# Optimization experiments

Hardware: AMD Instinct MI355X
Metric: run time of the kernel (lower is better)

Reference implementation:

```python
import jax, jax.numpy as jnp
import numpy as np

B, C_IN, C_TMP, C_OUT, N = 4, 256, 256, 256, 4096


def setup_inputs() -> dict:
    key = jax.random.key(0)
    k1, k2, k3, k4 = jax.random.split(key, 4)
    scale = 1.0 / np.sqrt(C_IN)
    return {
        "fea": jax.random.normal(k1, (B, C_IN, N), dtype=jnp.float32),
        "Wq": jax.random.normal(k2, (C_TMP, C_IN), dtype=jnp.float32) * scale,
        "Wk": jax.random.normal(k3, (C_TMP, C_IN), dtype=jnp.float32) * scale,
        "Wv": jax.random.normal(k4, (C_OUT, C_IN), dtype=jnp.float32) * scale,
    }


def reference(fea, Wq, Wk, Wv):
    # 1x1 Conv1d == per-point channel matmul
    Q = jnp.einsum("ti,bin->btn", Wq, fea)   # (B, temp, N)
    K = jnp.einsum("ti,bin->btn", Wk, fea)   # (B, temp, N)
    V = jnp.einsum("oi,bin->bon", Wv, fea)   # (B, out, N)
    # S[b, i, j] = sum_t K[b, t, i] * Q[b, t, j]; note: no 1/sqrt(d) scaling
    S = jnp.einsum("bti,btj->bij", K, Q)     # (B, N, N)
    S = jax.nn.softmax(S, axis=1)            # softmax over key axis (dim=1)
    new_fea = jnp.einsum("bok,bkn->bon", V, S)  # (B, out, N)
    # merge == 'concat'
    out = jnp.concatenate([new_fea, fea], axis=1)  # (B, out+in, N)
    return jax.nn.relu(out)
```

## Files before the change

### kernel.cpp

```cpp
#include <hip/hip_runtime.h>

#define NB 4
#define C  256
#define NN 4096
#define TAU 8.0f

typedef _Float16 half8   __attribute__((ext_vector_type(8)));
typedef _Float16 half4_t __attribute__((ext_vector_type(4)));
typedef float    f32x4   __attribute__((ext_vector_type(4)));

static __device__ __forceinline__ f32x4 mfma16(half8 a, half8 b, f32x4 c) {
    return __builtin_amdgcn_mfma_f32_16x16x32_f16(a, b, c, 0, 0, 0);
}

static __device__ __forceinline__ void gld16(const void* g, void* l) {
    __builtin_amdgcn_global_load_lds(
        (const __attribute__((address_space(1))) unsigned int*)g,
        (__attribute__((address_space(3))) unsigned int*)l, 16, 0, 0);
}

__global__ __launch_bounds__(256) void proj_kernel(
    const float* __restrict__ fea, const float* __restrict__ Wq,
    const float* __restrict__ Wk, const float* __restrict__ Wv,
    _Float16* __restrict__ Qt, _Float16* __restrict__ Kt,
    _Float16* __restrict__ Vp, float* __restrict__ out)
{
    const int lin = blockIdx.x + gridDim.x * blockIdx.y;
    const int xcd = lin & 7;
    const int b   = xcd >> 1;
    const int nt  = ((lin >> 3) << 1) | (xcd & 1);
    const int n0  = nt * 32;

    __shared__ __align__(16) _Float16 fh[32][264];
    __shared__ __align__(16) _Float16 fl[32][264];

    const int tid = threadIdx.x;
    {
        const int nl = tid & 31, rr = tid >> 5;
        const float* feab = fea + (size_t)b * C * NN + n0 + nl;
        float* outb = out + (size_t)b * 2 * C * NN + (size_t)C * NN + n0 + nl;
#pragma unroll
        for (int p = 0; p < 32; ++p) {
            const int i = p * 8 + rr;
            const float v = feab[(size_t)i * NN];
            outb[(size_t)i * NN] = fmaxf(v, 0.f);
            const _Float16 h = (_Float16)v;
            fh[nl][i] = h;
            fl[nl][i] = (_Float16)(v - (float)h);
        }
    }
    __syncthreads();

    const int w = tid >> 6, lane = tid & 63, lr = lane & 15, lg = lane >> 4;

    const float* const Ws[2] = {Wq, Wk};
    _Float16* const   Od[2] = {Qt + (size_t)b * NN * C, Kt + (size_t)b * NN * C};
#pragma unroll 1
    for (int qk = 0; qk < 2; ++qk) {
        const float* __restrict__ W = Ws[qk];
        f32x4 acc[2][4];
#pragma unroll
        for (int mi = 0; mi < 2; ++mi)
#pragma unroll
            for (int ni = 0; ni < 4; ++ni) acc[mi][ni] = (f32x4){0.f, 0.f, 0.f, 0.f};

#pragma unroll 1
        for (int kt = 0; kt < 8; ++kt) {
            half8 ah[2], al[2];
#pragma unroll
            for (int mi = 0; mi < 2; ++mi) {
                ah[mi] = *(const half8*)&fh[mi * 16 + lr][kt * 32 + lg * 8];
                al[mi] = *(const half8*)&fl[mi * 16 + lr][kt * 32 + lg * 8];
            }
            half8 bh[4], bl[4];
#pragma unroll
            for (int ni = 0; ni < 4; ++ni) {
                const float* src = W + (size_t)(w * 64 + ni * 16 + lr) * C + kt * 32 + lg * 8;
                const float4 x0 = *(const float4*)src;
                const float4 x1 = *(const float4*)(src + 4);
                const float xs[8] = {x0.x, x0.y, x0.z, x0.w, x1.x, x1.y, x1.z, x1.w};
#pragma unroll
                for (int e = 0; e < 8; ++e) {
                    const _Float16 h = (_Float16)xs[e];
                    bh[ni][e] = h;
                    bl[ni][e] = (_Float16)(xs[e] - (float)h);
                }
            }
#pragma unroll
            for (int mi = 0; mi < 2; ++mi)
#pragma unroll
                for (int ni = 0; ni < 4; ++ni) {
                    acc[mi][ni] = mfma16(ah[mi], bh[ni], acc[mi][ni]);
                    acc[mi][ni] = mfma16(ah[mi], bl[ni], acc[mi][ni]);
                    acc[mi][ni] = mfma16(al[mi], bh[ni], acc[mi][ni]);
                }
        }
        _Float16* dst = Od[qk];
#pragma unroll
        for (int mi = 0; mi < 2; ++mi)
#pragma unroll
            for (int ni = 0; ni < 4; ++ni)
#pragma unroll
                for (int r = 0; r < 4; ++r)
                    dst[(size_t)(n0 + mi * 16 + lg * 4 + r) * C + (w * 64 + ni * 16 + lr)] =
                        (_Float16)acc[mi][ni][r];
    }

    {
        f32x4 acc[4][2];
#pragma unroll
        for (int mi = 0; mi < 4; ++mi)
#pragma unroll
            for (int ni = 0; ni < 2; ++ni) acc[mi][ni] = (f32x4){0.f, 0.f, 0.f, 0.f};

#pragma unroll 1
        for (int kt = 0; kt < 8; ++kt) {
            half8 ah[4], al[4];
#pragma unroll
            for (int mi = 0; mi < 4; ++mi) {
                const float* src = Wv + (size_t)(w * 64 + mi * 16 + lr) * C + kt * 32 + lg * 8;
                const float4 x0 = *(const float4*)src;
                const float4 x1 = *(const float4*)(src + 4);
                const float xs[8] = {x0.x, x0.y, x0.z, x0.w, x1.x, x1.y, x1.z, x1.w};
#pragma unroll
                for (int e = 0; e < 8; ++e) {
                    const _Float16 h = (_Float16)xs[e];
                    ah[mi][e] = h;
                    al[mi][e] = (_Float16)(xs[e] - (float)h);
                }
            }
            half8 bh[2], bl[2];
#pragma unroll
            for (int ni = 0; ni < 2; ++ni) {
                bh[ni] = *(const half8*)&fh[ni * 16 + lr][kt * 32 + lg * 8];
                bl[ni] = *(const half8*)&fl[ni * 16 + lr][kt * 32 + lg * 8];
            }
#pragma unroll
            for (int mi = 0; mi < 4; ++mi)
#pragma unroll
                for (int ni = 0; ni < 2; ++ni) {
                    acc[mi][ni] = mfma16(ah[mi], bh[ni], acc[mi][ni]);
                    acc[mi][ni] = mfma16(ah[mi], bl[ni], acc[mi][ni]);
                    acc[mi][ni] = mfma16(al[mi], bh[ni], acc[mi][ni]);
                }
        }
        _Float16* vb = Vp + (size_t)b * C * NN;
#pragma unroll
        for (int mi = 0; mi < 4; ++mi)
#pragma unroll
            for (int ni = 0; ni < 2; ++ni)
#pragma unroll
                for (int r = 0; r < 4; ++r)
                    vb[(size_t)(w * 64 + mi * 16 + lg * 4 + r) * NN + n0 + ni * 16 + lr] =
                        (_Float16)acc[mi][ni][r];
    }
}


#define STAGE(nb, t) do {                                                      \
    char* kd = (char*)&Kb_s[nb][0];                                            \
    char* vd = (char*)&Vb_s[nb][0];                                            \
    const char* kt_ = Ktile0 + (size_t)(t) * 16384;                            \
    const char* vt_ = Vtile0 + (size_t)(t) * 64;                               \
    { const int ub = w * 1024; const int a = ub + lane * 16;                   \
      gld16(kt_ + (a ^ (((a >> 9) & 7) << 4)), kd + ub);                       \
      gld16(vt_ + ((size_t)(a >> 6) * 8192 +                                   \
                   ((a & 63) ^ (((a >> 6) & 3) << 4))), vd + ub); }            \
    { const int ub = (8 + w) * 1024; const int a = ub + lane * 16;             \
      gld16(kt_ + (a ^ (((a >> 9) & 7) << 4)), kd + ub);                       \
      gld16(vt_ + ((size_t)(a >> 6) * 8192 +                                   \
                   ((a & 63) ^ (((a >> 6) & 3) << 4))), vd + ub); }            \
} while (0)

template<int KS>
__global__ __launch_bounds__(512, 2) void attn_split(
    const _Float16* __restrict__ Qt, const _Float16* __restrict__ Kt,
    const _Float16* __restrict__ Vp, _Float16* __restrict__ Opart,
    float* __restrict__ ml, float* __restrict__ out)
{
    const int lin = blockIdx.x;
    const int xcd = lin & 7, slot = lin >> 3;
    int b, ks, jt;
    if constexpr (KS == 4) {
        const int combo = xcd * 2 + (slot >> 4);
        b = combo >> 2; ks = combo & 3; jt = slot & 15;
    } else if constexpr (KS == 2) {
        b = xcd >> 1; ks = xcd & 1; jt = slot;
    } else {
        b = xcd >> 1; ks = 0; jt = (slot << 1) | (xcd & 1);
    }

    const int tid = threadIdx.x;
    const int w = tid >> 6, lane = tid & 63, lr = lane & 15, lg = lane >> 4;
    const int j0 = jt * 256 + w * 32;
    const int T = (NN / KS) / 32;
    const int iBase = ks * (NN / KS);

    __shared__ __align__(16) _Float16 Kb_s[2][32 * 256];
    __shared__ __align__(16) _Float16 Vb_s[2][256 * 32];
    __shared__ __align__(16) _Float16 Pb_s[8][1024];

    const _Float16* Qb = Qt + (size_t)b * NN * C;
    const char* Ktile0 = (const char*)(Kt + (size_t)b * NN * C + (size_t)iBase * C);
    const char* Vtile0 = (const char*)(Vp + (size_t)b * C * NN + iBase);

    half8 q[2][8];
#pragma unroll
    for (int jn = 0; jn < 2; ++jn)
#pragma unroll
        for (int k8 = 0; k8 < 8; ++k8)
            q[jn][k8] = *(const half8*)(Qb + (size_t)(j0 + jn * 16 + lr) * C + k8 * 32 + lg * 8);

    f32x4 O[16][2];
#pragma unroll
    for (int oi = 0; oi < 16; ++oi) {
        O[oi][0] = (f32x4){0.f, 0.f, 0.f, 0.f};
        O[oi][1] = (f32x4){0.f, 0.f, 0.f, 0.f};
    }
    float m0 = -1e30f, m1 = -1e30f, l0 = 0.f, l1 = 0.f;

    const int kswzK = (lr & 7) << 4;
    const int kswzP = (lr & 3) << 4;

    STAGE(0, 0);
    __syncthreads();

    char* pw = (char*)&Pb_s[w][0];

#pragma unroll 1
    for (int t = 0; t < T; ++t) {
        const int cur = t & 1;
        if (t + 1 < T) STAGE(cur ^ 1, t + 1);

        const char* kb = (const char*)&Kb_s[cur][0];
        f32x4 s00 = (f32x4){0,0,0,0}, s01 = (f32x4){0,0,0,0};
        f32x4 s10 = (f32x4){0,0,0,0}, s11 = (f32x4){0,0,0,0};
#pragma unroll
        for (int k8 = 0; k8 < 8; ++k8) {
            const int cb = (k8 * 64 + lg * 16) ^ kswzK;
            const half8 a0 = *(const half8*)(kb + lr * 512 + cb);
            const half8 a1 = *(const half8*)(kb + (16 + lr) * 512 + cb);
            s00 = mfma16(a0, q[0][k8], s00);
            s10 = mfma16(a0, q[1][k8], s10);
            s01 = mfma16(a1, q[0][k8], s01);
            s11 = mfma16(a1, q[1][k8], s11);
        }

        float tm0 = fmaxf(fmaxf(fmaxf(s00[0], s00[1]), fmaxf(s00[2], s00[3])),
                          fmaxf(fmaxf(s01[0], s01[1]), fmaxf(s01[2], s01[3])));
        float tm1 = fmaxf(fmaxf(fmaxf(s10[0], s10[1]), fmaxf(s10[2], s10[3])),
                          fmaxf(fmaxf(s11[0], s11[1]), fmaxf(s11[2], s11[3])));
        tm0 = fmaxf(tm0, __shfl_xor(tm0, 16, 64));
        tm0 = fmaxf(tm0, __shfl_xor(tm0, 32, 64));
        tm1 = fmaxf(tm1, __shfl_xor(tm1, 16, 64));
        tm1 = fmaxf(tm1, __shfl_xor(tm1, 32, 64));
        if (__any((tm0 > m0 + TAU) || (tm1 > m1 + TAU))) {
            const float mn0 = fmaxf(m0, tm0), mn1 = fmaxf(m1, tm1);
            const float sc0 = __expf(m0 - mn0), sc1 = __expf(m1 - mn1);
            l0 *= sc0; l1 *= sc1; m0 = mn0; m1 = mn1;
#pragma unroll
            for (int oi = 0; oi < 16; ++oi) { O[oi][0] *= sc0; O[oi][1] *= sc1; }
        }

        float ss0 = 0.f, ss1 = 0.f;
#pragma unroll
        for (int mi = 0; mi < 2; ++mi) {
            const f32x4 sv = mi ? s01 : s00;
            half4_t ph;
#pragma unroll
            for (int r = 0; r < 4; ++r) {
                const float p = __expf(sv[r] - m0); ss0 += p; ph[r] = (_Float16)p;
            }
            *(half4_t*)(pw + lr * 64 + ((mi * 32 + lg * 8) ^ kswzP)) = ph;
        }
#pragma unroll
        for (int mi = 0; mi < 2; ++mi) {
            const f32x4 sv = mi ? s11 : s10;
            half4_t ph;
#pragma unroll
            for (int r = 0; r < 4; ++r) {
                const float p = __expf(sv[r] - m1); ss1 += p; ph[r] = (_Float16)p;
            }
            *(half4_t*)(pw + (16 + lr) * 64 + ((mi * 32 + lg * 8) ^ kswzP)) = ph;
        }
        ss0 += __shfl_xor(ss0, 16, 64); ss0 += __shfl_xor(ss0, 32, 64); l0 += ss0;
        ss1 += __shfl_xor(ss1, 16, 64); ss1 += __shfl_xor(ss1, 32, 64); l1 += ss1;

        asm volatile("s_waitcnt lgkmcnt(0)" ::: "memory");
        __builtin_amdgcn_sched_barrier(0);

        const half8 pf0 = *(const half8*)(pw + lr * 64 + ((lg * 16) ^ kswzP));
        const half8 pf1 = *(const half8*)(pw + (16 + lr) * 64 + ((lg * 16) ^ kswzP));
        const char* vb = (const char*)&Vb_s[cur][0];
#pragma unroll
        for (int oi = 0; oi < 16; ++oi) {
            const half8 vf = *(const half8*)(vb + (oi * 16 + lr) * 64 + ((lg * 16) ^ kswzP));
            O[oi][0] = mfma16(vf, pf0, O[oi][0]);
            O[oi][1] = mfma16(vf, pf1, O[oi][1]);
        }
        __syncthreads();
    }

    const float inv0 = 1.f / l0, inv1 = 1.f / l1;
    if constexpr (KS == 1) {
        float* ob = out + (size_t)b * 2 * C * NN;
#pragma unroll
        for (int oi = 0; oi < 16; ++oi)
#pragma unroll
            for (int r = 0; r < 4; ++r) {
                const int o = oi * 16 + lg * 4 + r;
                ob[(size_t)o * NN + j0 + lr]      = fmaxf(O[oi][0][r] * inv0, 0.f);
                ob[(size_t)o * NN + j0 + 16 + lr] = fmaxf(O[oi][1][r] * inv1, 0.f);
            }
    } else {
        _Float16* op = Opart + (size_t)(b * KS + ks) * C * NN;
#pragma unroll
        for (int oi = 0; oi < 16; ++oi)
#pragma unroll
            for (int r = 0; r < 4; ++r) {
                const int o = oi * 16 + lg * 4 + r;
                op[(size_t)o * NN + j0 + lr]      = (_Float16)(O[oi][0][r] * inv0);
                op[(size_t)o * NN + j0 + 16 + lr] = (_Float16)(O[oi][1][r] * inv1);
            }
        if (lg == 0) {
            float* mlb = ml + (size_t)(b * KS + ks) * 2 * NN;
            mlb[j0 + lr]          = m0;  mlb[j0 + 16 + lr]      = m1;
            mlb[NN + j0 + lr]     = l0;  mlb[NN + j0 + 16 + lr] = l1;
        }
    }
}

template<int KS>
__global__ __launch_bounds__(256) void combine_kernel(
    const _Float16* __restrict__ Opart, const float* __restrict__ ml,
    float* __restrict__ out)
{
    const int b = blockIdx.x >> 6, cc = blockIdx.x & 63;
    const int tid = threadIdx.x;
    const int col = cc * 64 + (tid & 63);
    const int op0 = tid >> 6;
    float mv[KS], wgt[KS];
    float M = -1e30f;
#pragma unroll
    for (int s = 0; s < KS; ++s) {
        mv[s] = ml[(size_t)(b * KS + s) * 2 * NN + col];
        M = fmaxf(M, mv[s]);
    }
    float L = 0.f;
#pragma unroll
    for (int s = 0; s < KS; ++s) {
        const float lv = ml[((size_t)(b * KS + s) * 2 + 1) * NN + col];
        wgt[s] = __expf(mv[s] - M) * lv; L += wgt[s];
    }
    const float invL = 1.f / L;
#pragma unroll
    for (int s = 0; s < KS; ++s) wgt[s] *= invL;
    float* ob = out + (size_t)b * 2 * C * NN + col;
    for (int oit = 0; oit < 64; ++oit) {
        const int o = oit * 4 + op0;
        float acc = 0.f;
#pragma unroll
        for (int s = 0; s < KS; ++s)
            acc += wgt[s] * (float)Opart[((size_t)(b * KS + s) * C + o) * NN + col];
        ob[(size_t)o * NN] = fmaxf(acc, 0.f);
    }
}

extern "C" void kernel_launch(void* const* d_in, const int* in_sizes, int n_in,
                              void* d_out, int out_size, void* d_ws, size_t ws_size,
                              hipStream_t stream) {
    const float* fea = (const float*)d_in[0];
    const float* Wq  = (const float*)d_in[1];
    const float* Wk  = (const float*)d_in[2];
    const float* Wv  = (const float*)d_in[3];
    float* out = (float*)d_out;

    _Float16* Qt = (_Float16*)d_ws;
    _Float16* Kt = Qt + (size_t)NB * NN * C;
    _Float16* Vp = Kt + (size_t)NB * NN * C;
    char* extra = (char*)(Vp + (size_t)NB * NN * C);
    const size_t base = (size_t)3 * NB * NN * C * sizeof(_Float16);

    proj_kernel<<<dim3(128, 4), 256, 0, stream>>>(fea, Wq, Wk, Wv, Qt, Kt, Vp, out);

    const size_t need4 = base + (size_t)4 * NB * C * NN * 2 + (size_t)4 * NB * 2 * NN * 4;
    const size_t need2 = base + (size_t)2 * NB * C * NN * 2 + (size_t)2 * NB * 2 * NN * 4;

    if (ws_size >= need4) {
        _Float16* Op = (_Float16*)extra;
        float* mlp = (float*)(extra + (size_t)4 * NB * C * NN * 2);
        attn_split<4><<<256, 512, 0, stream>>>(Qt, Kt, Vp, Op, mlp, out);
        combine_kernel<4><<<NB * 64, 256, 0, stream>>>(Op, mlp, out);
    } else if (ws_size >= need2) {
        _Float16* Op = (_Float16*)extra;
        float* mlp = (float*)(extra + (size_t)2 * NB * C * NN * 2);
        attn_split<2><<<128, 512, 0, stream>>>(Qt, Kt, Vp, Op, mlp, out);
        combine_kernel<2><<<NB * 64, 256, 0, stream>>>(Op, mlp, out);
    } else {
        attn_split<1><<<64, 512, 0, stream>>>(Qt, Kt, Vp, nullptr, nullptr, out);
    }
}
```

Before: 153.9 us.

## Drop split-fp16 projections and rewrite attention with 32x32 MFMA and fp16 accumulators

```diff
diff --git a/kernel.cpp b/kernel.cpp
--- a/kernel.cpp
+++ b/kernel.cpp
@@ -3,20 +3,27 @@
 #define NB 4
 #define C  256
 #define NN 4096
-#define TAU 8.0f
 
 typedef _Float16 half8   __attribute__((ext_vector_type(8)));
 typedef _Float16 half4_t __attribute__((ext_vector_type(4)));
+typedef _Float16 h2      __attribute__((ext_vector_type(2)));
 typedef float    f32x4   __attribute__((ext_vector_type(4)));
+typedef float    f32x16  __attribute__((ext_vector_type(16)));
 
 static __device__ __forceinline__ f32x4 mfma16(half8 a, half8 b, f32x4 c) {
     return __builtin_amdgcn_mfma_f32_16x16x32_f16(a, b, c, 0, 0, 0);
 }
-
+static __device__ __forceinline__ f32x16 mfma32(half8 a, half8 b, f32x16 c) {
+    return __builtin_amdgcn_mfma_f32_32x32x16_f16(a, b, c, 0, 0, 0);
+}
 static __device__ __forceinline__ void gld16(const void* g, void* l) {
     __builtin_amdgcn_global_load_lds(
         (const __attribute__((address_space(1))) unsigned int*)g,
         (__attribute__((address_space(3))) unsigned int*)l, 16, 0, 0);
+}
+static __device__ __forceinline__ h2 cvtpk(float a, float b) {
+    auto r = __builtin_amdgcn_cvt_pkrtz(a, b);
+    return *reinterpret_cast<h2*>(&r);
 }
 
 __global__ __launch_bounds__(256) void proj_kernel(
@@ -32,7 +39,6 @@
     const int n0  = nt * 32;
 
     __shared__ __align__(16) _Float16 fh[32][264];
-    __shared__ __align__(16) _Float16 fl[32][264];
 
     const int tid = threadIdx.x;
     {
@@ -44,9 +50,7 @@
             const int i = p * 8 + rr;
             const float v = feab[(size_t)i * NN];
             outb[(size_t)i * NN] = fmaxf(v, 0.f);
-            const _Float16 h = (_Float16)v;
-            fh[nl][i] = h;
-            fl[nl][i] = (_Float16)(v - (float)h);
+            fh[nl][i] = (_Float16)v;
         }
     }
     __syncthreads();
@@ -66,34 +70,26 @@
 
 #pragma unroll 1
         for (int kt = 0; kt < 8; ++kt) {
-            half8 ah[2], al[2];
-#pragma unroll
-            for (int mi = 0; mi < 2; ++mi) {
+            half8 ah[2];
+#pragma unroll
+            for (int mi = 0; mi < 2; ++mi)
                 ah[mi] = *(const half8*)&fh[mi * 16 + lr][kt * 32 + lg * 8];
-                al[mi] = *(const half8*)&fl[mi * 16 + lr][kt * 32 + lg * 8];
-            }
-            half8 bh[4], bl[4];
+            half8 bh[4];
 #pragma unroll
             for (int ni = 0; ni < 4; ++ni) {
                 const float* src = W + (size_t)(w * 64 + ni * 16 + lr) * C + kt * 32 + lg * 8;
                 const float4 x0 = *(const float4*)src;
                 const float4 x1 = *(const float4*)(src + 4);
-                const float xs[8] = {x0.x, x0.y, x0.z, x0.w, x1.x, x1.y, x1.z, x1.w};
-#pragma unroll
-                for (int e = 0; e < 8; ++e) {
-                    const _Float16 h = (_Float16)xs[e];
-                    bh[ni][e] = h;
-                    bl[ni][e] = (_Float16)(xs[e] - (float)h);
-                }
+                bh[ni][0] = (_Float16)x0.x; bh[ni][1] = (_Float16)x0.y;
+                bh[ni][2] = (_Float16)x0.z; bh[ni][3] = (_Float16)x0.w;
+                bh[ni][4] = (_Float16)x1.x; bh[ni][5] = (_Float16)x1.y;
+                bh[ni][6] = (_Float16)x1.z; bh[ni][7] = (_Float16)x1.w;
             }
 #pragma unroll
             for (int mi = 0; mi < 2; ++mi)
 #pragma unroll
-                for (int ni = 0; ni < 4; ++ni) {
+                for (int ni = 0; ni < 4; ++ni)
                     acc[mi][ni] = mfma16(ah[mi], bh[ni], acc[mi][ni]);
-                    acc[mi][ni] = mfma16(ah[mi], bl[ni], acc[mi][ni]);
-                    acc[mi][ni] = mfma16(al[mi], bh[ni], acc[mi][ni]);
-                }
         }
         _Float16* dst = Od[qk];
 #pragma unroll
@@ -115,34 +111,26 @@
 
 #pragma unroll 1
         for (int kt = 0; kt < 8; ++kt) {
-            half8 ah[4], al[4];
+            half8 ah[4];
 #pragma unroll
             for (int mi = 0; mi < 4; ++mi) {
                 const float* src = Wv + (size_t)(w * 64 + mi * 16 + lr) * C + kt * 32 + lg * 8;
                 const float4 x0 = *(const float4*)src;
                 const float4 x1 = *(const float4*)(src + 4);
-                const float xs[8] = {x0.x, x0.y, x0.z, x0.w, x1.x, x1.y, x1.z, x1.w};
-#pragma unroll
-                for (int e = 0; e < 8; ++e) {
-                    const _Float16 h = (_Float16)xs[e];
-                    ah[mi][e] = h;
-                    al[mi][e] = (_Float16)(xs[e] - (float)h);
-                }
-            }
-            half8 bh[2], bl[2];
-#pragma unroll
-            for (int ni = 0; ni < 2; ++ni) {
+                ah[mi][0] = (_Float16)x0.x; ah[mi][1] = (_Float16)x0.y;
+                ah[mi][2] = (_Float16)x0.z; ah[mi][3] = (_Float16)x0.w;
+                ah[mi][4] = (_Float16)x1.x; ah[mi][5] = (_Float16)x1.y;
+                ah[mi][6] = (_Float16)x1.z; ah[mi][7] = (_Float16)x1.w;
+            }
+            half8 bh[2];
+#pragma unroll
+            for (int ni = 0; ni < 2; ++ni)
                 bh[ni] = *(const half8*)&fh[ni * 16 + lr][kt * 32 + lg * 8];
-                bl[ni] = *(const half8*)&fl[ni * 16 + lr][kt * 32 + lg * 8];
-            }
 #pragma unroll
             for (int mi = 0; mi < 4; ++mi)
 #pragma unroll
-                for (int ni = 0; ni < 2; ++ni) {
+                for (int ni = 0; ni < 2; ++ni)
                     acc[mi][ni] = mfma16(ah[mi], bh[ni], acc[mi][ni]);
-                    acc[mi][ni] = mfma16(ah[mi], bl[ni], acc[mi][ni]);
-                    acc[mi][ni] = mfma16(al[mi], bh[ni], acc[mi][ni]);
-                }
         }
         _Float16* vb = Vp + (size_t)b * C * NN;
 #pragma unroll
@@ -156,178 +144,227 @@
     }
 }
 
-
-#define STAGE(nb, t) do {                                                      \
-    char* kd = (char*)&Kb_s[nb][0];                                            \
-    char* vd = (char*)&Vb_s[nb][0];                                            \
-    const char* kt_ = Ktile0 + (size_t)(t) * 16384;                            \
-    const char* vt_ = Vtile0 + (size_t)(t) * 64;                               \
-    { const int ub = w * 1024; const int a = ub + lane * 16;                   \
-      gld16(kt_ + (a ^ (((a >> 9) & 7) << 4)), kd + ub);                       \
-      gld16(vt_ + ((size_t)(a >> 6) * 8192 +                                   \
-                   ((a & 63) ^ (((a >> 6) & 3) << 4))), vd + ub); }            \
-    { const int ub = (8 + w) * 1024; const int a = ub + lane * 16;             \
-      gld16(kt_ + (a ^ (((a >> 9) & 7) << 4)), kd + ub);                       \
-      gld16(vt_ + ((size_t)(a >> 6) * 8192 +                                   \
-                   ((a & 63) ^ (((a >> 6) & 3) << 4))), vd + ub); }            \
-} while (0)
-
 template<int KS>
-__global__ __launch_bounds__(512, 2) void attn_split(
+__global__ __launch_bounds__(512, 2) void attn2(
     const _Float16* __restrict__ Qt, const _Float16* __restrict__ Kt,
     const _Float16* __restrict__ Vp, _Float16* __restrict__ Opart,
     float* __restrict__ ml, float* __restrict__ out)
 {
+    extern __shared__ char smem[];
+    char* Ksh = smem;
+    char* Vsh0 = smem + 32768;
+    char* Vsh1 = smem + 65536;
+    char* Psh = smem + 98304;
+    float* stats = (float*)(smem + 131072);
+
     const int lin = blockIdx.x;
     const int xcd = lin & 7, slot = lin >> 3;
-    int b, ks, jt;
-    if constexpr (KS == 4) {
-        const int combo = xcd * 2 + (slot >> 4);
-        b = combo >> 2; ks = combo & 3; jt = slot & 15;
-    } else if constexpr (KS == 2) {
-        b = xcd >> 1; ks = xcd & 1; jt = slot;
-    } else {
-        b = xcd >> 1; ks = 0; jt = (slot << 1) | (xcd & 1);
-    }
+    int b, ksid, jt;
+    if constexpr (KS == 4) { b = xcd >> 1; ksid = ((xcd & 1) << 1) | (slot >> 4); jt = slot & 15; }
+    else                   { b = xcd >> 1; ksid = 0; jt = (slot << 1) | (xcd & 1); }
 
     const int tid = threadIdx.x;
-    const int w = tid >> 6, lane = tid & 63, lr = lane & 15, lg = lane >> 4;
-    const int j0 = jt * 256 + w * 32;
-    const int T = (NN / KS) / 32;
-    const int iBase = ks * (NN / KS);
-
-    __shared__ __align__(16) _Float16 Kb_s[2][32 * 256];
-    __shared__ __align__(16) _Float16 Vb_s[2][256 * 32];
-    __shared__ __align__(16) _Float16 Pb_s[8][1024];
+    const int w = tid >> 6, lane = tid & 63;
+    const int g = w >> 2, jg = w & 3;
+    const int l31 = lane & 31, hi = lane >> 5, lr = lane & 15, lg = lane >> 4;
+    const int j0 = jt * 256 + jg * 64;
+    const int iBase = ksid * (NN / KS);
+    const int T = (NN / KS) / 64;
 
     const _Float16* Qb = Qt + (size_t)b * NN * C;
-    const char* Ktile0 = (const char*)(Kt + (size_t)b * NN * C + (size_t)iBase * C);
-    const char* Vtile0 = (const char*)(Vp + (size_t)b * C * NN + iBase);
-
-    half8 q[2][8];
-#pragma unroll
-    for (int jn = 0; jn < 2; ++jn)
-#pragma unroll
-        for (int k8 = 0; k8 < 8; ++k8)
-            q[jn][k8] = *(const half8*)(Qb + (size_t)(j0 + jn * 16 + lr) * C + k8 * 32 + lg * 8);
-
-    f32x4 O[16][2];
-#pragma unroll
-    for (int oi = 0; oi < 16; ++oi) {
-        O[oi][0] = (f32x4){0.f, 0.f, 0.f, 0.f};
-        O[oi][1] = (f32x4){0.f, 0.f, 0.f, 0.f};
-    }
-    float m0 = -1e30f, m1 = -1e30f, l0 = 0.f, l1 = 0.f;
-
-    const int kswzK = (lr & 7) << 4;
-    const int kswzP = (lr & 3) << 4;
-
-    STAGE(0, 0);
-    __syncthreads();
-
-    char* pw = (char*)&Pb_s[w][0];
+    const char* KbC = (const char*)(Kt + (size_t)b * NN * C);
+    const char* VbC = (const char*)(Vp + (size_t)b * C * NN);
+
+    const int swzA = (l31 & 7) << 4;
+    const int swzB = (lr & 7) << 4;
+
+    half8 q[2][16];
+#pragma unroll
+    for (int jf = 0; jf < 2; ++jf)
+#pragma unroll
+        for (int kk = 0; kk < 16; ++kk)
+            q[jf][kk] = *(const half8*)(Qb + (size_t)(j0 + jf * 32 + l31) * C + kk * 16 + hi * 8);
+
+    h2 Om[8][4][2];
+#pragma unroll
+    for (int of = 0; of < 8; ++of)
+#pragma unroll
+        for (int c = 0; c < 4; ++c) { Om[of][c][0] = (h2){0, 0}; Om[of][c][1] = (h2){0, 0}; }
+    float mrq[2] = {-1e30f, -1e30f};
+    float mrp[4] = {-1e30f, -1e30f, -1e30f, -1e30f};
+    float ll[2] = {0.f, 0.f};
+
+#define STAGE(dstV, t_) do {                                                   \
+    const int i0_ = iBase + (t_) * 64;                                         \
+    const char* ksg_ = KbC + (size_t)i0_ * 512;                                \
+    _Pragma("unroll")                                                          \
+    for (int r_ = 0; r_ < 4; ++r_) {                                           \
+        const int p_ = r_ * 8192 + tid * 16;                                   \
+        const int row_ = p_ >> 9, col_ = p_ & 511;                             \
+        gld16(ksg_ + (size_t)row_ * 512 + (col_ ^ ((row_ & 7) << 4)), Ksh + p_); \
+    }                                                                          \
+    _Pragma("unroll")                                                          \
+    for (int r_ = 0; r_ < 4; ++r_) {                                           \
+        const int p_ = r_ * 8192 + tid * 16;                                   \
+        const int row_ = p_ >> 7, col_ = p_ & 127;                             \
+        gld16(VbC + (size_t)row_ * 8192 + (size_t)i0_ * 2 + (col_ ^ ((row_ & 7) << 4)), (dstV) + p_); \
+    }                                                                          \
+} while (0)
+
+    STAGE(Vsh0, 0);
 
 #pragma unroll 1
     for (int t = 0; t < T; ++t) {
-        const int cur = t & 1;
-        if (t + 1 < T) STAGE(cur ^ 1, t + 1);
-
-        const char* kb = (const char*)&Kb_s[cur][0];
-        f32x4 s00 = (f32x4){0,0,0,0}, s01 = (f32x4){0,0,0,0};
-        f32x4 s10 = (f32x4){0,0,0,0}, s11 = (f32x4){0,0,0,0};
-#pragma unroll
-        for (int k8 = 0; k8 < 8; ++k8) {
-            const int cb = (k8 * 64 + lg * 16) ^ kswzK;
-            const half8 a0 = *(const half8*)(kb + lr * 512 + cb);
-            const half8 a1 = *(const half8*)(kb + (16 + lr) * 512 + cb);
-            s00 = mfma16(a0, q[0][k8], s00);
-            s10 = mfma16(a0, q[1][k8], s10);
-            s01 = mfma16(a1, q[0][k8], s01);
-            s11 = mfma16(a1, q[1][k8], s11);
-        }
-
-        float tm0 = fmaxf(fmaxf(fmaxf(s00[0], s00[1]), fmaxf(s00[2], s00[3])),
-                          fmaxf(fmaxf(s01[0], s01[1]), fmaxf(s01[2], s01[3])));
-        float tm1 = fmaxf(fmaxf(fmaxf(s10[0], s10[1]), fmaxf(s10[2], s10[3])),
-                          fmaxf(fmaxf(s11[0], s11[1]), fmaxf(s11[2], s11[3])));
-        tm0 = fmaxf(tm0, __shfl_xor(tm0, 16, 64));
-        tm0 = fmaxf(tm0, __shfl_xor(tm0, 32, 64));
-        tm1 = fmaxf(tm1, __shfl_xor(tm1, 16, 64));
-        tm1 = fmaxf(tm1, __shfl_xor(tm1, 32, 64));
-        if (__any((tm0 > m0 + TAU) || (tm1 > m1 + TAU))) {
-            const float mn0 = fmaxf(m0, tm0), mn1 = fmaxf(m1, tm1);
-            const float sc0 = __expf(m0 - mn0), sc1 = __expf(m1 - mn1);
-            l0 *= sc0; l1 *= sc1; m0 = mn0; m1 = mn1;
-#pragma unroll
-            for (int oi = 0; oi < 16; ++oi) { O[oi][0] *= sc0; O[oi][1] *= sc1; }
-        }
-
-        float ss0 = 0.f, ss1 = 0.f;
-#pragma unroll
-        for (int mi = 0; mi < 2; ++mi) {
-            const f32x4 sv = mi ? s01 : s00;
-            half4_t ph;
-#pragma unroll
-            for (int r = 0; r < 4; ++r) {
-                const float p = __expf(sv[r] - m0); ss0 += p; ph[r] = (_Float16)p;
-            }
-            *(half4_t*)(pw + lr * 64 + ((mi * 32 + lg * 8) ^ kswzP)) = ph;
-        }
-#pragma unroll
-        for (int mi = 0; mi < 2; ++mi) {
-            const f32x4 sv = mi ? s11 : s10;
-            half4_t ph;
-#pragma unroll
-            for (int r = 0; r < 4; ++r) {
-                const float p = __expf(sv[r] - m1); ss1 += p; ph[r] = (_Float16)p;
-            }
-            *(half4_t*)(pw + (16 + lr) * 64 + ((mi * 32 + lg * 8) ^ kswzP)) = ph;
-        }
-        ss0 += __shfl_xor(ss0, 16, 64); ss0 += __shfl_xor(ss0, 32, 64); l0 += ss0;
-        ss1 += __shfl_xor(ss1, 16, 64); ss1 += __shfl_xor(ss1, 32, 64); l1 += ss1;
-
-        asm volatile("s_waitcnt lgkmcnt(0)" ::: "memory");
+        __syncthreads();
+
+        f32x16 s[2];
+        s[0] = (f32x16)(0.f); s[1] = (f32x16)(0.f);
+        const char* krow = Ksh + (size_t)(g * 32 + l31) * 512;
+#pragma unroll
+        for (int kk = 0; kk < 16; ++kk) {
+            const half8 a = *(const half8*)(krow + ((kk * 32 + hi * 16) ^ swzA));
+            s[0] = mfma32(a, q[0][kk], s[0]);
+            s[1] = mfma32(a, q[1][kk], s[1]);
+        }
+
+#pragma unroll
+        for (int jf = 0; jf < 2; ++jf) {
+            float mh = s[jf][0];
+#pragma unroll
+            for (int r = 1; r < 16; ++r) mh = fmaxf(mh, s[jf][r]);
+            mh = fmaxf(mh, __shfl_xor(mh, 32, 64));
+            if (hi == 0) stats[(jg * 2 + g) * 64 + jf * 32 + l31] = mh;
+        }
+        __syncthreads();
+
+        if (t + 1 < T) {
+            if ((t + 1) & 1) STAGE(Vsh1, t + 1); else STAGE(Vsh0, t + 1);
+        }
+
+        float scq[2];
+#pragma unroll
+        for (int jf = 0; jf < 2; ++jf) {
+            const int j = jf * 32 + l31;
+            const float mt = fmaxf(stats[(jg * 2 + 0) * 64 + j], stats[(jg * 2 + 1) * 64 + j]);
+            const float mn = fmaxf(mrq[jf], mt);
+            scq[jf] = __expf(mrq[jf] - mn);
+            mrq[jf] = mn;
+            ll[jf] *= scq[jf];
+        }
+#pragma unroll
+        for (int c = 0; c < 4; ++c) {
+            const int j = c * 16 + lr;
+            const float mt = fmaxf(stats[(jg * 2 + 0) * 64 + j], stats[(jg * 2 + 1) * 64 + j]);
+            const float mn = fmaxf(mrp[c], mt);
+            const float sc = __expf(mrp[c] - mn);
+            mrp[c] = mn;
+            const h2 s2 = {(_Float16)sc, (_Float16)sc};
+#pragma unroll
+            for (int of = 0; of < 8; ++of) { Om[of][c][0] *= s2; Om[of][c][1] *= s2; }
+        }
+
+        char* pw = Psh + jg * 8192;
+#pragma unroll
+        for (int jf = 0; jf < 2; ++jf) {
+            const int jl = jf * 32 + l31;
+            float lsum = 0.f;
+#pragma unroll
+            for (int qc = 0; qc < 4; ++qc) {
+                half4_t ph;
+#pragma unroll
+                for (int r = 0; r < 4; ++r) {
+                    const float p = __expf(s[jf][qc * 4 + r] - mrq[jf]);
+                    lsum += p;
+                    ph[r] = (_Float16)p;
+                }
+                *(half4_t*)(pw + (size_t)jl * 128 + ((qc * 16 + hi * 8 + g * 64) ^ swzA)) = ph;
+            }
+            ll[jf] += lsum;
+        }
+
+        asm volatile("s_waitcnt lgkmcnt(0)\n\ts_barrier" ::: "memory");
         __builtin_amdgcn_sched_barrier(0);
 
-        const half8 pf0 = *(const half8*)(pw + lr * 64 + ((lg * 16) ^ kswzP));
-        const half8 pf1 = *(const half8*)(pw + (16 + lr) * 64 + ((lg * 16) ^ kswzP));
-        const char* vb = (const char*)&Vb_s[cur][0];
-#pragma unroll
-        for (int oi = 0; oi < 16; ++oi) {
-            const half8 vf = *(const half8*)(vb + (oi * 16 + lr) * 64 + ((lg * 16) ^ kswzP));
-            O[oi][0] = mfma16(vf, pf0, O[oi][0]);
-            O[oi][1] = mfma16(vf, pf1, O[oi][1]);
-        }
-        __syncthreads();
-    }
-
-    const float inv0 = 1.f / l0, inv1 = 1.f / l1;
-    if constexpr (KS == 1) {
+        const char* vB = ((t & 1) ? Vsh1 : Vsh0);
+        const char* pr = Psh + jg * 8192;
+#pragma unroll
+        for (int kk = 0; kk < 2; ++kk) {
+            half8 pb[4];
+#pragma unroll
+            for (int c = 0; c < 4; ++c)
+                pb[c] = *(const half8*)(pr + (size_t)(c * 16 + lr) * 128 + ((kk * 64 + lg * 16) ^ swzB));
+#pragma unroll
+            for (int of = 0; of < 8; ++of) {
+                const int vrow = g * 128 + of * 16 + lr;
+                const half8 va = *(const half8*)(vB + (size_t)vrow * 128 + ((kk * 64 + lg * 16) ^ swzB));
+#pragma unroll
+                for (int c = 0; c < 4; ++c) {
+                    f32x4 acc = (f32x4){0.f, 0.f, 0.f, 0.f};
+                    acc = mfma16(va, pb[c], acc);
+                    Om[of][c][0] += cvtpk(acc[0], acc[1]);
+                    Om[of][c][1] += cvtpk(acc[2], acc[3]);
+                }
+            }
+        }
+    }
+
+    __syncthreads();
+#pragma unroll
+    for (int jf = 0; jf < 2; ++jf) {
+        float lt = ll[jf] + __shfl_xor(ll[jf], 32, 64);
+        if (hi == 0) stats[(jg * 2 + g) * 64 + jf * 32 + l31] = lt;
+    }
+    __syncthreads();
+
+    float il[4];
+#pragma unroll
+    for (int c = 0; c < 4; ++c) {
+        const int j = c * 16 + lr;
+        const float L = stats[(jg * 2 + 0) * 64 + j] + stats[(jg * 2 + 1) * 64 + j];
+        il[c] = 1.f / L;
+    }
+
+    if constexpr (KS == 4) {
+        if (g == 0 && hi == 0) {
+            float* mlb = ml + (size_t)(b * KS + ksid) * 2 * NN;
+#pragma unroll
+            for (int jf = 0; jf < 2; ++jf) {
+                const int j = jf * 32 + l31;
+                const float L = stats[(jg * 2 + 0) * 64 + j] + stats[(jg * 2 + 1) * 64 + j];
+                mlb[j0 + j] = mrq[jf];
+                mlb[NN + j0 + j] = L;
+            }
+        }
+        _Float16* op = Opart + (size_t)(b * KS + ksid) * C * NN;
+#pragma unroll
+        for (int of = 0; of < 8; ++of)
+#pragma unroll
+            for (int c = 0; c < 4; ++c) {
+                const int o0 = g * 128 + of * 16 + lg * 4;
+                const int j = j0 + c * 16 + lr;
+                const h2 ih = {(_Float16)il[c], (_Float16)il[c]};
+                const h2 v0 = Om[of][c][0] * ih;
+                const h2 v1 = Om[of][c][1] * ih;
+                op[(size_t)(o0 + 0) * NN + j] = v0[0];
+                op[(size_t)(o0 + 1) * NN + j] = v0[1];
+                op[(size_t)(o0 + 2) * NN + j] = v1[0];
+                op[(size_t)(o0 + 3) * NN + j] = v1[1];
+            }
+    } else {
         float* ob = out + (size_t)b * 2 * C * NN;
 #pragma unroll
-        for (int oi = 0; oi < 16; ++oi)
-#pragma unroll
-            for (int r = 0; r < 4; ++r) {
-                const int o = oi * 16 + lg * 4 + r;
-                ob[(size_t)o * NN + j0 + lr]      = fmaxf(O[oi][0][r] * inv0, 0.f);
-                ob[(size_t)o * NN + j0 + 16 + lr] = fmaxf(O[oi][1][r] * inv1, 0.f);
-            }
-    } else {
-        _Float16* op = Opart + (size_t)(b * KS + ks) * C * NN;
-#pragma unroll
-        for (int oi = 0; oi < 16; ++oi)
-#pragma unroll
-            for (int r = 0; r < 4; ++r) {
-                const int o = oi * 16 + lg * 4 + r;
-                op[(size_t)o * NN + j0 + lr]      = (_Float16)(O[oi][0][r] * inv0);
-                op[(size_t)o * NN + j0 + 16 + lr] = (_Float16)(O[oi][1][r] * inv1);
-            }
-        if (lg == 0) {
-            float* mlb = ml + (size_t)(b * KS + ks) * 2 * NN;
-            mlb[j0 + lr]          = m0;  mlb[j0 + 16 + lr]      = m1;
-            mlb[NN + j0 + lr]     = l0;  mlb[NN + j0 + 16 + lr] = l1;
-        }
-    }
+        for (int of = 0; of < 8; ++of)
+#pragma unroll
+            for (int c = 0; c < 4; ++c) {
+                const int o0 = g * 128 + of * 16 + lg * 4;
+                const int j = j0 + c * 16 + lr;
+                ob[(size_t)(o0 + 0) * NN + j] = fmaxf((float)Om[of][c][0][0] * il[c], 0.f);
+                ob[(size_t)(o0 + 1) * NN + j] = fmaxf((float)Om[of][c][0][1] * il[c], 0.f);
+                ob[(size_t)(o0 + 2) * NN + j] = fmaxf((float)Om[of][c][1][0] * il[c], 0.f);
+                ob[(size_t)(o0 + 3) * NN + j] = fmaxf((float)Om[of][c][1][1] * il[c], 0.f);
+            }
+    }
+#undef STAGE
 }
 
 template<int KS>
@@ -383,20 +420,19 @@
 
     proj_kernel<<<dim3(128, 4), 256, 0, stream>>>(fea, Wq, Wk, Wv, Qt, Kt, Vp, out);
 
+    const int SMEM = 131072 + 2048;
     const size_t need4 = base + (size_t)4 * NB * C * NN * 2 + (size_t)4 * NB * 2 * NN * 4;
-    const size_t need2 = base + (size_t)2 * NB * C * NN * 2 + (size_t)2 * NB * 2 * NN * 4;
 
     if (ws_size >= need4) {
         _Float16* Op = (_Float16*)extra;
         float* mlp = (float*)(extra + (size_t)4 * NB * C * NN * 2);
-        attn_split<4><<<256, 512, 0, stream>>>(Qt, Kt, Vp, Op, mlp, out);
+        (void)hipFuncSetAttribute(reinterpret_cast<const void*>(&attn2<4>),
+                                  hipFuncAttributeMaxDynamicSharedMemorySize, SMEM);
+        attn2<4><<<256, 512, SMEM, stream>>>(Qt, Kt, Vp, Op, mlp, out);
         combine_kernel<4><<<NB * 64, 256, 0, stream>>>(Op, mlp, out);
-    } else if (ws_size >= need2) {
-        _Float16* Op = (_Float16*)extra;
-        float* mlp = (float*)(extra + (size_t)2 * NB * C * NN * 2);
-        attn_split<2><<<128, 512, 0, stream>>>(Qt, Kt, Vp, Op, mlp, out);
-        combine_kernel<2><<<NB * 64, 256, 0, stream>>>(Op, mlp, out);
     } else {
-        attn_split<1><<<64, 512, 0, stream>>>(Qt, Kt, Vp, nullptr, nullptr, out);
-    }
-}
+        (void)hipFuncSetAttribute(reinterpret_cast<const void*>(&attn2<1>),
+                                  hipFuncAttributeMaxDynamicSharedMemorySize, SMEM);
+        attn2<1><<<64, 512, SMEM, stream>>>(Qt, Kt, Vp, nullptr, nullptr, out);
+    }
+}
```

Result: slower. 256.5 us (+66.7%).
